# Performance work log

Measured on AMD Instinct MI355X. Metric: run time of the kernel, lower is better.

## Reference

```python
import jax, jax.numpy as jnp
import numpy as np

HEADS = 8
N_NODES = 16384
DIM = 256
NUM_GLOBAL = 4
E_LOCAL = 131072
E_EXP = 65536


def setup_inputs() -> dict:
    key = jax.random.key(0)
    ks = jax.random.split(key, 8)
    x = jax.random.normal(ks[0], (N_NODES, DIM), dtype=jnp.float32)
    edge_index = jax.random.randint(ks[1], (2, E_LOCAL), 0, N_NODES)
    expander_edge_index = jax.random.randint(ks[2], (2, E_EXP), 0, N_NODES)
    W_qkv = jax.random.normal(ks[3], (DIM, 3 * DIM), dtype=jnp.float32) * (DIM ** -0.5)
    b_qkv = jax.random.normal(ks[4], (3 * DIM,), dtype=jnp.float32) * 0.01
    W_out = jax.random.normal(ks[5], (DIM, DIM), dtype=jnp.float32) * (DIM ** -0.5)
    b_out = jax.random.normal(ks[6], (DIM,), dtype=jnp.float32) * 0.01
    global_tokens = jax.random.normal(ks[7], (NUM_GLOBAL, DIM), dtype=jnp.float32)
    return {"x": x, "edge_index": edge_index,
            "expander_edge_index": expander_edge_index,
            "W_qkv": W_qkv, "b_qkv": b_qkv,
            "W_out": W_out, "b_out": b_out,
            "global_tokens": global_tokens}


def _build_edges(edge_index, expander_edge_index, N, G):
    # local edges + self loops (PyG add_self_loops appends [i,i] edges)
    self_loops = jnp.arange(N)
    nodes = jnp.arange(N)
    gids = jnp.arange(N, N + G)
    # node -> global: meshgrid(arange(N), global_nodes, 'ij') -> src node repeated, dst global tiled
    n2g_src = jnp.repeat(nodes, G)
    n2g_dst = jnp.tile(gids, N)
    src = jnp.concatenate([edge_index[0], self_loops, expander_edge_index[0], n2g_src, n2g_dst])
    dst = jnp.concatenate([edge_index[1], self_loops, expander_edge_index[1], n2g_dst, n2g_src])
    return src, dst


def reference(x, edge_index, expander_edge_index, W_qkv, b_qkv, W_out, b_out, global_tokens):
    N, dim = x.shape
    G = global_tokens.shape[0]
    H = HEADS
    D = dim // H
    total = N + G

    x_full = jnp.concatenate([x, global_tokens], axis=0)          # [N+G, dim]
    qkv = (x_full @ W_qkv + b_qkv).reshape(total, 3, H, D)
    Q, K, V = qkv[:, 0], qkv[:, 1], qkv[:, 2]                     # [N+G, H, D]

    src, dst = _build_edges(edge_index, expander_edge_index, N, G)  # [E]

    scale = D ** -0.5
    scores = (Q[dst] * K[src]).sum(axis=-1) * scale               # [E, H]

    # segment softmax over destination nodes
    m = jax.ops.segment_max(scores, dst, num_segments=total)      # [N+G, H]
    e = jnp.exp(scores - m[dst])                                  # [E, H]
    denom = jax.ops.segment_sum(e, dst, num_segments=total)       # [N+G, H]
    attn = e / denom[dst]                                         # [E, H]

    # scatter-weighted V sum (index_add over dst)
    out = jax.ops.segment_sum(attn[:, :, None] * V[src], dst, num_segments=total)  # [N+G, H, D]
    out = out[:N].reshape(N, H * D)
    return out @ W_out + b_out
```

## Files before the change

### kernel.cpp

```cpp
#include <hip/hip_runtime.h>
#include <hip/hip_bf16.h>
#include <stdint.h>

#define N_NODES   16384
#define DIMM      256
#define HEADS     8
#define HDIM      32
#define NUM_GLOBAL 4
#define N_TOT     (N_NODES + NUM_GLOBAL)
#define E_LOCAL   131072
#define E_EXP     65536
#define E_CSR     (E_LOCAL + E_EXP)
#define ADJ_CAP   64

typedef __hip_bfloat16 bf16;
typedef __attribute__((ext_vector_type(8))) short short8;
typedef __attribute__((ext_vector_type(4))) short sh4;
typedef __attribute__((ext_vector_type(4))) float f32x4;

__device__ __forceinline__ short f2s(float f) {
    bf16 h = __float2bfloat16(f);
    return __builtin_bit_cast(short, h);
}
__device__ __forceinline__ float bu2f(unsigned short u) {
    return __bfloat162float(__builtin_bit_cast(bf16, u));
}

__device__ __forceinline__ int swz(int c, int r) {
    return c ^ (r & 7) ^ ((r >> 3) & 7);
}

__global__ __launch_bounds__(256) void prep_kernel(
    const float* __restrict__ Wqkv, const float* __restrict__ Wout,
    const int* __restrict__ ei, const int* __restrict__ xei,
    const float* __restrict__ x, const float* __restrict__ gtok,
    bf16* __restrict__ Wt1, bf16* __restrict__ Wt2,
    int* __restrict__ cnt, unsigned short* __restrict__ adjP, bf16* __restrict__ Xb)
{
    const int b = blockIdx.x;
    const int t = threadIdx.x;
    if (b < 64) {
        __shared__ float T[64][65];
        const float* src; bf16* dst; int n0, k0, ldn;
        if (b < 48) { src = Wqkv; dst = Wt1; n0 = (b % 12) * 64; k0 = (b / 12) * 64; ldn = 768; }
        else        { int bb = b - 48; src = Wout; dst = Wt2; n0 = (bb & 3) * 64; k0 = (bb >> 2) * 64; ldn = 256; }
        #pragma unroll
        for (int i = 0; i < 4; ++i) {
            int idx = t + 256 * i;
            int r = idx >> 4, c4 = (idx & 15) * 4;
            float4 v = *(const float4*)(src + (size_t)(k0 + r) * ldn + n0 + c4);
            T[r][c4] = v.x; T[r][c4 + 1] = v.y; T[r][c4 + 2] = v.z; T[r][c4 + 3] = v.w;
        }
        __syncthreads();
        #pragma unroll
        for (int i = 0; i < 4; ++i) {
            int idx = t + 256 * i;
            int nr = idx >> 4, kk = (idx & 15) * 4;
            sh4 o;
            o[0] = f2s(T[kk][nr]);     o[1] = f2s(T[kk + 1][nr]);
            o[2] = f2s(T[kk + 2][nr]); o[3] = f2s(T[kk + 3][nr]);
            *(sh4*)(dst + (size_t)(n0 + nr) * 256 + k0 + kk) = o;
        }
    } else if (b < 832) {
        int e = (b - 64) * 256 + t;
        int s, d;
        if (e < E_LOCAL)      { s = ei[e];            d = ei[E_LOCAL + e]; }
        else if (e < E_CSR)   { int ee = e - E_LOCAL; s = xei[ee]; d = xei[E_EXP + ee]; }
        else return;
        int pos = atomicAdd(&cnt[d], 1);
        if (pos < ADJ_CAP) adjP[(d << 6) + pos] = (unsigned short)s;
    } else {
        int e0 = ((b - 832) * 256 + t) * 8;
        if (e0 < N_TOT * DIMM) {
            int row = e0 >> 8, col = e0 & 255;
            const float* p = (row < N_NODES)
                ? x + (size_t)row * DIMM + col
                : gtok + (size_t)(row - N_NODES) * DIMM + col;
            float4 v0 = *(const float4*)p, v1 = *(const float4*)(p + 4);
            short8 o;
            o[0] = f2s(v0.x); o[1] = f2s(v0.y); o[2] = f2s(v0.z); o[3] = f2s(v0.w);
            o[4] = f2s(v1.x); o[5] = f2s(v1.y); o[6] = f2s(v1.z); o[7] = f2s(v1.w);
            *(short8*)((short*)Xb + (size_t)row * DIMM + col) = o;
        }
    }
}

__global__ __launch_bounds__(256) void qkv_mfma(
    const bf16* __restrict__ Xb, const bf16* __restrict__ Wt,
    const float* __restrict__ bias,
    bf16* __restrict__ Qb, bf16* __restrict__ KVb)
{
    const int b = blockIdx.x;
    const int xcd = b & 7;
    const int i = b >> 3;
    const int mt = xcd + 8 * (i / 6);
    if (mt >= 129) return;
    const int m0 = mt * 128;
    const int n0 = (i % 6) * 128;

    __shared__ __align__(16) short SM[32768];
    const int t  = threadIdx.x;
    const int wid = t >> 6, lane = t & 63;
    const int wr = wid >> 1, wc = wid & 1;
    const int lm = lane & 15, lq = lane >> 4;

    f32x4 acc[4][4] = {};
    short8 aregs[4];

    int sr[4], skc[4];
    #pragma unroll
    for (int ii = 0; ii < 4; ++ii) {
        int c8 = t + 256 * ii;
        sr[ii] = c8 >> 3; skc[ii] = c8 & 7;
    }

    #pragma unroll
    for (int ii = 0; ii < 4; ++ii)
        aregs[ii] = *(const short8*)((const short*)Xb + (size_t)(m0 + sr[ii]) * DIMM + skc[ii] * 8);
    #pragma unroll
    for (int ii = 0; ii < 4; ++ii)
        *(short8*)(SM + sr[ii] * 64 + swz(skc[ii], sr[ii]) * 8) = aregs[ii];
    #pragma unroll
    for (int ii = 0; ii < 4; ++ii) {
        short8 v = *(const short8*)((const short*)Wt + (size_t)(n0 + sr[ii]) * 256 + skc[ii] * 8);
        *(short8*)(SM + 8192 + sr[ii] * 64 + swz(skc[ii], sr[ii]) * 8) = v;
    }
    __syncthreads();

    #pragma unroll
    for (int tstep = 0; tstep < 4; ++tstep) {
        const int p = tstep & 1;
        short* As = SM + p * 16384;
        short* Bs = As + 8192;
        if (tstep < 3) {
            const int kn = (tstep + 1) * 64;
            #pragma unroll
            for (int ii = 0; ii < 4; ++ii)
                aregs[ii] = *(const short8*)((const short*)Xb + (size_t)(m0 + sr[ii]) * DIMM + kn + skc[ii] * 8);
        }
        #pragma unroll
        for (int kk = 0; kk < 2; ++kk) {
            const int c = kk * 4 + lq;
            short8 af[4], bfq[4];
            #pragma unroll
            for (int mi = 0; mi < 4; ++mi) {
                int r = wr * 64 + mi * 16 + lm;
                af[mi] = *(const short8*)(As + r * 64 + swz(c, r) * 8);
            }
            #pragma unroll
            for (int ni = 0; ni < 4; ++ni) {
                int n = wc * 64 + ni * 16 + lm;
                bfq[ni] = *(const short8*)(Bs + n * 64 + swz(c, n) * 8);
            }
            #pragma unroll
            for (int mi = 0; mi < 4; ++mi)
                #pragma unroll
                for (int ni = 0; ni < 4; ++ni)
                    acc[mi][ni] = __builtin_amdgcn_mfma_f32_16x16x32_bf16(
                        af[mi], bfq[ni], acc[mi][ni], 0, 0, 0);
        }
        if (tstep < 3) {
            const int kn = (tstep + 1) * 64;
            short* An = SM + (1 - p) * 16384;
            short* Bn = An + 8192;
            __syncthreads();
            #pragma unroll
            for (int ii = 0; ii < 4; ++ii)
                *(short8*)(An + sr[ii] * 64 + swz(skc[ii], sr[ii]) * 8) = aregs[ii];
            #pragma unroll
            for (int ii = 0; ii < 4; ++ii) {
                short8 v = *(const short8*)((const short*)Wt + (size_t)(n0 + sr[ii]) * 256 + kn + skc[ii] * 8);
                *(short8*)(Bn + sr[ii] * 64 + swz(skc[ii], sr[ii]) * 8) = v;
            }
            __syncthreads();
        }
    }

    __syncthreads();
    #pragma unroll
    for (int ni = 0; ni < 4; ++ni) {
        int col = wc * 64 + ni * 16 + lm;
        float bv = bias[n0 + col];
        #pragma unroll
        for (int mi = 0; mi < 4; ++mi) {
            int rowb = wr * 64 + mi * 16 + lq * 4;
            #pragma unroll
            for (int rr = 0; rr < 4; ++rr)
                SM[(rowb + rr) * 136 + col] = f2s(acc[mi][ni][rr] + bv);
        }
    }
    __syncthreads();
    #pragma unroll
    for (int it = 0; it < 8; ++it) {
        int idx = it * 256 + t;
        int r = idx >> 4, c8 = idx & 15;
        int row = m0 + r;
        if (row < N_TOT) {
            int colbase = n0 + (c8 >> 3) * 64;
            int sel = colbase >> 8;
            int cc = (colbase & 255) + (c8 & 7) * 8;
            short8 v = *(const short8*)(SM + r * 136 + c8 * 8);
            short* dp;
            if (sel == 0) dp = (short*)Qb + (size_t)row * DIMM + cc;
            else          dp = (short*)KVb + (size_t)row * 512 + (sel - 1) * 256 + cc;
            *(short8*)dp = v;
        }
    }
}

__global__ __launch_bounds__(256) void out_mfma(
    const bf16* __restrict__ O, const bf16* __restrict__ Wt,
    const float* __restrict__ bias, float* __restrict__ out)
{
    const int b = blockIdx.x;
    const int xcd = b & 7;
    const int i = b >> 3;
    const int m0 = (xcd + 8 * (i >> 1)) * 128;
    const int n0 = (i & 1) * 128;

    __shared__ __align__(16) short SM[128 * 136];
    short* As = SM;
    short* Bs = SM + 128 * 64;
    float* CF = (float*)SM;
    const int t  = threadIdx.x;
    const int wid = t >> 6, lane = t & 63;
    const int wr = wid >> 1, wc = wid & 1;
    const int lm = lane & 15, lq = lane >> 4;

    f32x4 acc[4][4] = {};

    for (int k0 = 0; k0 < DIMM; k0 += 64) {
        if (k0) __syncthreads();
        #pragma unroll
        for (int ii = 0; ii < 4; ++ii) {
            int c8 = t + 256 * ii;
            int r  = c8 >> 3, kc = c8 & 7;
            short8 v = *(const short8*)((const short*)O + (size_t)(m0 + r) * DIMM + k0 + kc * 8);
            *(short8*)(As + r * 64 + swz(kc, r) * 8) = v;
        }
        #pragma unroll
        for (int ii = 0; ii < 4; ++ii) {
            int c8 = t + 256 * ii;
            int n  = c8 >> 3, kc = c8 & 7;
            short8 v = *(const short8*)((const short*)Wt + (size_t)(n0 + n) * 256 + k0 + kc * 8);
            *(short8*)(Bs + n * 64 + swz(kc, n) * 8) = v;
        }
        __syncthreads();
        #pragma unroll
        for (int kk = 0; kk < 2; ++kk) {
            const int c = kk * 4 + lq;
            short8 af[4], bfq[4];
            #pragma unroll
            for (int mi = 0; mi < 4; ++mi) {
                int r = wr * 64 + mi * 16 + lm;
                af[mi] = *(const short8*)(As + r * 64 + swz(c, r) * 8);
            }
            #pragma unroll
            for (int ni = 0; ni < 4; ++ni) {
                int n = wc * 64 + ni * 16 + lm;
                bfq[ni] = *(const short8*)(Bs + n * 64 + swz(c, n) * 8);
            }
            #pragma unroll
            for (int mi = 0; mi < 4; ++mi)
                #pragma unroll
                for (int ni = 0; ni < 4; ++ni)
                    acc[mi][ni] = __builtin_amdgcn_mfma_f32_16x16x32_bf16(
                        af[mi], bfq[ni], acc[mi][ni], 0, 0, 0);
        }
    }

    #pragma unroll
    for (int p = 0; p < 2; ++p) {
        __syncthreads();
        if (wr == p) {
            #pragma unroll
            for (int ni = 0; ni < 4; ++ni) {
                int col = wc * 64 + ni * 16 + lm;
                float bv = bias[n0 + col];
                #pragma unroll
                for (int mi = 0; mi < 4; ++mi) {
                    int lr = mi * 16 + lq * 4;
                    #pragma unroll
                    for (int rr = 0; rr < 4; ++rr) {
                        float val = acc[mi][ni][rr] + bv;
                        val = fminf(fmaxf(val, -1e4f), 1e4f);
                        CF[(lr + rr) * 132 + col] = val;
                    }
                }
            }
        }
        __syncthreads();
        #pragma unroll
        for (int it = 0; it < 8; ++it) {
            int idx = it * 256 + t;
            int r = idx >> 5, c4 = idx & 31;
            float4 v = *(const float4*)(CF + r * 132 + c4 * 4);
            *(float4*)(out + (size_t)(m0 + p * 64 + r) * DIMM + n0 + c4 * 4) = v;
        }
    }
}

__global__ __launch_bounds__(256) void attn_kernel(
    const bf16* __restrict__ Qb, const bf16* __restrict__ KVb,
    const int* __restrict__ cnt, const unsigned short* __restrict__ adjP,
    bf16* __restrict__ Ob)
{
    const int wave = (blockIdx.x * blockDim.x + threadIdx.x) >> 6;
    const int lane = threadIdx.x & 63;
    if (wave >= N_NODES) return;
    const int n = wave;
    const float scale = 0.1767766952966369f;

    const ushort4* KV4 = (const ushort4*)KVb;

    ushort4 qu = ((const ushort4*)Qb)[(size_t)n * 64 + lane];
    float4 q;
    q.x = bu2f(qu.x) * scale; q.y = bu2f(qu.y) * scale;
    q.z = bu2f(qu.z) * scale; q.w = bu2f(qu.w) * scale;

    const int areg = adjP[(n << 6) + lane];

    const int deg = min(cnt[n], ADJ_CAP);
    const int tot = deg + 5;

    float4 acc = make_float4(0.f, 0.f, 0.f, 0.f);
    float dsum = 0.f;

    int svA[8], svB[8];
    float okA[8], okB[8];
    ushort4 kA[8], vA[8], kB[8], vB[8];

    auto IDX = [&](int base, int* sv, float* ok) {
        #pragma unroll
        for (int u = 0; u < 8; ++u) {
            int ii = base + u - 5;
            bool val = (ii < deg);
            int sg = __shfl(areg, ii & 63);
            int s  = (ii < 0) ? ((ii == -5) ? n : (N_NODES + ii + 4)) : sg;
            sv[u] = val ? s : n;
            ok[u] = val ? 1.f : 0.f;
        }
    };
    auto LOAD = [&](const int* sv, ushort4* kk, ushort4* vv) {
        #pragma unroll
        for (int u = 0; u < 8; ++u) kk[u] = KV4[(size_t)sv[u] * 128 + lane];
        #pragma unroll
        for (int u = 0; u < 8; ++u) vv[u] = KV4[(size_t)sv[u] * 128 + 64 + lane];
    };
    auto PROC = [&](const ushort4* kk, const ushort4* vv, const float* ok) {
        float p[8];
        #pragma unroll
        for (int u = 0; u < 8; ++u)
            p[u] = q.x * bu2f(kk[u].x) + q.y * bu2f(kk[u].y)
                 + q.z * bu2f(kk[u].z) + q.w * bu2f(kk[u].w);
        #pragma unroll
        for (int u = 0; u < 8; ++u) {
            p[u] += __shfl_xor(p[u], 1);
            p[u] += __shfl_xor(p[u], 2);
            p[u] += __shfl_xor(p[u], 4);
        }
        #pragma unroll
        for (int u = 0; u < 8; ++u) {
            float wgt = ok[u] * __expf(fminf(p[u], 80.f));
            dsum += wgt;
            acc.x += wgt * bu2f(vv[u].x);
            acc.y += wgt * bu2f(vv[u].y);
            acc.z += wgt * bu2f(vv[u].z);
            acc.w += wgt * bu2f(vv[u].w);
        }
    };

    IDX(0, svA, okA); LOAD(svA, kA, vA);
    int base = 0;
    while (true) {
        if (base + 8 < tot) { IDX(base + 8, svB, okB); LOAD(svB, kB, vB); }
        PROC(kA, vA, okA);
        if (base + 8 >= tot) break;
        if (base + 16 < tot) { IDX(base + 16, svA, okA); LOAD(svA, kA, vA); }
        PROC(kB, vB, okB);
        if (base + 16 >= tot) break;
        base += 16;
    }

    float r = 1.0f / fmaxf(dsum, 1e-30f);
    ushort4 o;
    o.x = (unsigned short)__builtin_bit_cast(short, __float2bfloat16(fminf(fmaxf(acc.x * r, -500.f), 500.f)));
    o.y = (unsigned short)__builtin_bit_cast(short, __float2bfloat16(fminf(fmaxf(acc.y * r, -500.f), 500.f)));
    o.z = (unsigned short)__builtin_bit_cast(short, __float2bfloat16(fminf(fmaxf(acc.z * r, -500.f), 500.f)));
    o.w = (unsigned short)__builtin_bit_cast(short, __float2bfloat16(fminf(fmaxf(acc.w * r, -500.f), 500.f)));
    ((ushort4*)Ob)[(size_t)n * 64 + lane] = o;
}

extern "C" void kernel_launch(void* const* d_in, const int* in_sizes, int n_in,
                              void* d_out, int out_size, void* d_ws, size_t ws_size,
                              hipStream_t stream)
{
    const float* x    = (const float*)d_in[0];
    const int*   ei   = (const int*)d_in[1];
    const int*   xei  = (const int*)d_in[2];
    const float* Wqkv = (const float*)d_in[3];
    const float* bqkv = (const float*)d_in[4];
    const float* Wout = (const float*)d_in[5];
    const float* bout = (const float*)d_in[6];
    const float* gtok = (const float*)d_in[7];

    int* cnt  = (int*)d_ws;
    unsigned short* adjP = (unsigned short*)(cnt + N_NODES);
    uintptr_t fb = ((uintptr_t)(adjP + (size_t)N_NODES * ADJ_CAP) + 15) & ~(uintptr_t)15;
    bf16*  Qb  = (bf16*)fb;
    bf16*  KVb = Qb + (size_t)N_TOT * DIMM;
    bf16*  Ob  = KVb + (size_t)N_TOT * 512;
    bf16*  Wt1 = Ob + (size_t)N_NODES * DIMM;
    bf16*  Wt2 = Wt1 + 768 * 256;
    bf16*  Xb  = Wt2 + 256 * 256;

    hipMemsetAsync(cnt, 0, N_NODES * sizeof(int), stream);

    prep_kernel<<<2881, 256, 0, stream>>>(Wqkv, Wout, ei, xei, x, gtok, Wt1, Wt2, cnt, adjP, Xb);
    qkv_mfma<<<816, 256, 0, stream>>>(Xb, Wt1, bqkv, Qb, KVb);
    attn_kernel<<<N_NODES / 4, 256, 0, stream>>>(Qb, KVb, cnt, adjP, Ob);
    out_mfma<<<256, 256, 0, stream>>>(Ob, Wt2, bout, (float*)d_out);
}
```

Baseline: 148.7 us.

## Store K/V head-major and process attention per head with 8 edges per wave

Result: slower. 158.5 us (+6.6%).

```diff
diff --git a/kernel.cpp b/kernel.cpp
--- a/kernel.cpp
+++ b/kernel.cpp
@@ -88,7 +88,7 @@
 __global__ __launch_bounds__(256) void qkv_mfma(
     const bf16* __restrict__ Xb, const bf16* __restrict__ Wt,
     const float* __restrict__ bias,
-    bf16* __restrict__ Qb, bf16* __restrict__ KVb)
+    bf16* __restrict__ Qb, bf16* __restrict__ KVh)
 {
     const int b = blockIdx.x;
     const int xcd = b & 7;
@@ -201,8 +201,12 @@
             int cc = (colbase & 255) + (c8 & 7) * 8;
             short8 v = *(const short8*)(SM + r * 136 + c8 * 8);
             short* dp;
-            if (sel == 0) dp = (short*)Qb + (size_t)row * DIMM + cc;
-            else          dp = (short*)KVb + (size_t)row * 512 + (sel - 1) * 256 + cc;
+            if (sel == 0) {
+                dp = (short*)Qb + (size_t)row * DIMM + cc;
+            } else {
+                int head = cc >> 5, dim = cc & 31;
+                dp = (short*)KVh + ((size_t)head * N_TOT + row) * 64 + (sel - 1) * 32 + dim;
+            }
             *(short8*)dp = v;
         }
     }
@@ -301,94 +305,91 @@
 }
 
 __global__ __launch_bounds__(256) void attn_kernel(
-    const bf16* __restrict__ Qb, const bf16* __restrict__ KVb,
+    const bf16* __restrict__ Qb, const bf16* __restrict__ KVh,
     const int* __restrict__ cnt, const unsigned short* __restrict__ adjP,
     bf16* __restrict__ Ob)
 {
-    const int wave = (blockIdx.x * blockDim.x + threadIdx.x) >> 6;
+    const int b = blockIdx.x;
+    const int head = b & 7;
+    const int wid = threadIdx.x >> 6;
     const int lane = threadIdx.x & 63;
-    if (wave >= N_NODES) return;
-    const int n = wave;
+    const int n = (b >> 3) * 4 + wid;
+    const int g = lane >> 3, j = lane & 7;
     const float scale = 0.1767766952966369f;
 
-    const ushort4* KV4 = (const ushort4*)KVb;
-
-    ushort4 qu = ((const ushort4*)Qb)[(size_t)n * 64 + lane];
+    const ushort4* KV4 = (const ushort4*)KVh + (size_t)head * N_TOT * 16;
+
+    ushort4 qu = ((const ushort4*)Qb)[(size_t)n * 64 + head * 8 + j];
     float4 q;
     q.x = bu2f(qu.x) * scale; q.y = bu2f(qu.y) * scale;
     q.z = bu2f(qu.z) * scale; q.w = bu2f(qu.w) * scale;
 
     const int areg = adjP[(n << 6) + lane];
-
     const int deg = min(cnt[n], ADJ_CAP);
     const int tot = deg + 5;
 
     float4 acc = make_float4(0.f, 0.f, 0.f, 0.f);
     float dsum = 0.f;
 
-    int svA[8], svB[8];
-    float okA[8], okB[8];
-    ushort4 kA[8], vA[8], kB[8], vB[8];
-
-    auto IDX = [&](int base, int* sv, float* ok) {
-        #pragma unroll
-        for (int u = 0; u < 8; ++u) {
-            int ii = base + u - 5;
-            bool val = (ii < deg);
-            int sg = __shfl(areg, ii & 63);
-            int s  = (ii < 0) ? ((ii == -5) ? n : (N_NODES + ii + 4)) : sg;
-            sv[u] = val ? s : n;
-            ok[u] = val ? 1.f : 0.f;
-        }
+    auto IDX = [&](int base, int& sv, float& ok) {
+        int ii = base + g - 5;
+        bool val = (ii < deg);
+        int sg = __shfl(areg, ii & 63);
+        int s  = (ii < 0) ? ((ii == -5) ? n : (N_NODES + ii + 4)) : sg;
+        sv = val ? s : n;
+        ok = val ? 1.f : 0.f;
     };
-    auto LOAD = [&](const int* sv, ushort4* kk, ushort4* vv) {
-        #pragma unroll
-        for (int u = 0; u < 8; ++u) kk[u] = KV4[(size_t)sv[u] * 128 + lane];
-        #pragma unroll
-        for (int u = 0; u < 8; ++u) vv[u] = KV4[(size_t)sv[u] * 128 + 64 + lane];
-    };
-    auto PROC = [&](const ushort4* kk, const ushort4* vv, const float* ok) {
-        float p[8];
-        #pragma unroll
-        for (int u = 0; u < 8; ++u)
-            p[u] = q.x * bu2f(kk[u].x) + q.y * bu2f(kk[u].y)
-                 + q.z * bu2f(kk[u].z) + q.w * bu2f(kk[u].w);
-        #pragma unroll
-        for (int u = 0; u < 8; ++u) {
-            p[u] += __shfl_xor(p[u], 1);
-            p[u] += __shfl_xor(p[u], 2);
-            p[u] += __shfl_xor(p[u], 4);
-        }
-        #pragma unroll
-        for (int u = 0; u < 8; ++u) {
-            float wgt = ok[u] * __expf(fminf(p[u], 80.f));
-            dsum += wgt;
-            acc.x += wgt * bu2f(vv[u].x);
-            acc.y += wgt * bu2f(vv[u].y);
-            acc.z += wgt * bu2f(vv[u].z);
-            acc.w += wgt * bu2f(vv[u].w);
-        }
-    };
-
-    IDX(0, svA, okA); LOAD(svA, kA, vA);
+
+    int svA; float okA;
+    IDX(0, svA, okA);
+    ushort4 kA = KV4[(size_t)svA * 16 + j];
+    ushort4 vA = KV4[(size_t)svA * 16 + 8 + j];
+
     int base = 0;
     while (true) {
-        if (base + 8 < tot) { IDX(base + 8, svB, okB); LOAD(svB, kB, vB); }
-        PROC(kA, vA, okA);
-        if (base + 8 >= tot) break;
-        if (base + 16 < tot) { IDX(base + 16, svA, okA); LOAD(svA, kA, vA); }
-        PROC(kB, vB, okB);
-        if (base + 16 >= tot) break;
-        base += 16;
-    }
-
-    float r = 1.0f / fmaxf(dsum, 1e-30f);
-    ushort4 o;
-    o.x = (unsigned short)__builtin_bit_cast(short, __float2bfloat16(fminf(fmaxf(acc.x * r, -500.f), 500.f)));
-    o.y = (unsigned short)__builtin_bit_cast(short, __float2bfloat16(fminf(fmaxf(acc.y * r, -500.f), 500.f)));
-    o.z = (unsigned short)__builtin_bit_cast(short, __float2bfloat16(fminf(fmaxf(acc.z * r, -500.f), 500.f)));
-    o.w = (unsigned short)__builtin_bit_cast(short, __float2bfloat16(fminf(fmaxf(acc.w * r, -500.f), 500.f)));
-    ((ushort4*)Ob)[(size_t)n * 64 + lane] = o;
+        int svB; float okB; ushort4 kB, vB;
+        const bool more = (base + 8 < tot);
+        if (more) {
+            IDX(base + 8, svB, okB);
+            kB = KV4[(size_t)svB * 16 + j];
+            vB = KV4[(size_t)svB * 16 + 8 + j];
+        }
+        {
+            float p = q.x * bu2f(kA.x) + q.y * bu2f(kA.y)
+                    + q.z * bu2f(kA.z) + q.w * bu2f(kA.w);
+            p += __shfl_xor(p, 1);
+            p += __shfl_xor(p, 2);
+            p += __shfl_xor(p, 4);
+            float wgt = okA * __expf(fminf(p, 80.f));
+            dsum += wgt;
+            acc.x += wgt * bu2f(vA.x);
+            acc.y += wgt * bu2f(vA.y);
+            acc.z += wgt * bu2f(vA.z);
+            acc.w += wgt * bu2f(vA.w);
+        }
+        if (!more) break;
+        base += 8;
+        svA = svB; okA = okB; kA = kB; vA = vB;
+    }
+
+    #pragma unroll
+    for (int m = 8; m <= 32; m <<= 1) {
+        acc.x += __shfl_xor(acc.x, m);
+        acc.y += __shfl_xor(acc.y, m);
+        acc.z += __shfl_xor(acc.z, m);
+        acc.w += __shfl_xor(acc.w, m);
+        dsum  += __shfl_xor(dsum, m);
+    }
+
+    if (lane < 8) {
+        float r = 1.0f / fmaxf(dsum, 1e-30f);
+        ushort4 o;
+        o.x = (unsigned short)__builtin_bit_cast(short, __float2bfloat16(fminf(fmaxf(acc.x * r, -500.f), 500.f)));
+        o.y = (unsigned short)__builtin_bit_cast(short, __float2bfloat16(fminf(fmaxf(acc.y * r, -500.f), 500.f)));
+        o.z = (unsigned short)__builtin_bit_cast(short, __float2bfloat16(fminf(fmaxf(acc.z * r, -500.f), 500.f)));
+        o.w = (unsigned short)__builtin_bit_cast(short, __float2bfloat16(fminf(fmaxf(acc.w * r, -500.f), 500.f)));
+        ((ushort4*)Ob)[(size_t)n * 64 + head * 8 + j] = o;
+    }
 }
 
 extern "C" void kernel_launch(void* const* d_in, const int* in_sizes, int n_in,
@@ -408,8 +409,8 @@
     unsigned short* adjP = (unsigned short*)(cnt + N_NODES);
     uintptr_t fb = ((uintptr_t)(adjP + (size_t)N_NODES * ADJ_CAP) + 15) & ~(uintptr_t)15;
     bf16*  Qb  = (bf16*)fb;
-    bf16*  KVb = Qb + (size_t)N_TOT * DIMM;
-    bf16*  Ob  = KVb + (size_t)N_TOT * 512;
+    bf16*  KVh = Qb + (size_t)N_TOT * DIMM;
+    bf16*  Ob  = KVh + (size_t)N_TOT * 512;
     bf16*  Wt1 = Ob + (size_t)N_NODES * DIMM;
     bf16*  Wt2 = Wt1 + 768 * 256;
     bf16*  Xb  = Wt2 + 256 * 256;
@@ -417,7 +418,7 @@
     hipMemsetAsync(cnt, 0, N_NODES * sizeof(int), stream);
 
     prep_kernel<<<2881, 256, 0, stream>>>(Wqkv, Wout, ei, xei, x, gtok, Wt1, Wt2, cnt, adjP, Xb);
-    qkv_mfma<<<816, 256, 0, stream>>>(Xb, Wt1, bqkv, Qb, KVb);
-    attn_kernel<<<N_NODES / 4, 256, 0, stream>>>(Qb, KVb, cnt, adjP, Ob);
+    qkv_mfma<<<816, 256, 0, stream>>>(Xb, Wt1, bqkv, Qb, KVh);
+    attn_kernel<<<(N_NODES / 4) * 8, 256, 0, stream>>>(Qb, KVh, cnt, adjP, Ob);
     out_mfma<<<256, 256, 0, stream>>>(Ob, Wt2, bout, (float*)d_out);
 }
```
